# Optimization experiments

Hardware: AMD Instinct MI355X
Metric: run time of the kernel (lower is better)

## Reference

```python
import jax, jax.numpy as jnp
import numpy as np


def setup_inputs() -> dict:
    key = jax.random.key(0)
    k1, k2 = jax.random.split(key)
    N, D, C = 65536, 512, 64
    embeddings = jax.random.normal(k1, (N, D), dtype=jnp.float32)
    labels = jax.random.randint(k2, (N,), 0, C, dtype=jnp.int64)
    return {"embeddings": embeddings, "labels": labels, "num_classes": C}


def reference(embeddings, labels, num_classes):
    # Per-class mean (prototypes) via segment reductions. Labels are assumed
    # to be 0..C-1 with all classes present, so unique(labels) == arange(C)
    # and local_labels == labels (faithful to the torch loop in that regime).
    ones = jnp.ones(labels.shape, dtype=embeddings.dtype)
    counts = jax.ops.segment_sum(ones, labels, num_segments=num_classes)  # [C]
    sums = jax.ops.segment_sum(embeddings, labels, num_segments=num_classes)  # [C, D]
    prototypes = sums / counts[:, None]

    # Euclidean cdist: ||e||^2 + ||p||^2 - 2 e.p^T, clamped for numerical safety
    e2 = jnp.sum(embeddings * embeddings, axis=1, keepdims=True)  # [N, 1]
    p2 = jnp.sum(prototypes * prototypes, axis=1)  # [C]
    cross = embeddings @ prototypes.T  # [N, C]
    d2 = jnp.maximum(e2 + p2[None, :] - 2.0 * cross, 1e-12)
    logits = -jnp.sqrt(d2)  # [N, C], negative distances

    log_probs = jax.nn.log_softmax(logits, axis=1)
    n = labels.shape[0]
    nll = -log_probs[jnp.arange(n), labels]
    loss = jnp.mean(nll)
    accuracy = jnp.mean((jnp.argmax(logits, axis=1) == labels).astype(jnp.float32))
    return (loss, accuracy)
```

## Files before the change

kernel.cpp:

```cpp
#include <hip/hip_runtime.h>
#include <math.h>

#define NROWS 65536
#define DIM   512
#define NCLS  64
#define CCAP  1280

typedef __attribute__((ext_vector_type(4))) float f32x4;
typedef __attribute__((ext_vector_type(8))) short s16x8;

#define WS_PROTOSUM 0
#define WS_CURSORS  32768
#define WS_LOSS     32832
#define WS_ACC      32833
#define WS_DONE     32834
#define WS_P2       32836
#define WS_PERM     32912
#define WS_PBF      114944
#define MEMSET_WORDS 32835

static __device__ __forceinline__ unsigned short f2bf(float f) {
    unsigned int u = __float_as_uint(f);
    u += 0x7FFF + ((u >> 16) & 1);
    return (unsigned short)(u >> 16);
}
static __device__ __forceinline__ float bf2f(unsigned short h) {
    return __uint_as_float(((unsigned int)h) << 16);
}

__global__ __launch_bounds__(256) void k_scatter(const int* __restrict__ labels,
                                                 int* __restrict__ cursors,
                                                 int* __restrict__ perm) {
    __shared__ int lh[NCLS], lb[NCLS];
    int t = threadIdx.x;
    if (t < NCLS) lh[t] = 0;
    __syncthreads();
    int i = blockIdx.x * 256 + t;
    int lab = labels[i];
    int rank = atomicAdd(&lh[lab], 1);
    __syncthreads();
    if (t < NCLS) lb[t] = atomicAdd(&cursors[t], lh[t]);
    __syncthreads();
    int pos = lb[lab] + rank;
    if (pos < CCAP) perm[lab * CCAP + pos] = i;
}

__global__ __launch_bounds__(256) void k_psum(const float* __restrict__ emb,
                                              const int* __restrict__ cursors,
                                              const int* __restrict__ perm,
                                              float* __restrict__ protoSum) {
    __shared__ int permS[CCAP];
    __shared__ float4 red[256];
    int t   = threadIdx.x;
    int c   = blockIdx.x >> 5;
    int sub = blockIdx.x & 31;
    int dc  = sub & 3;
    int rs  = sub >> 2;
    int tl  = t & 31;
    int g   = t >> 5;

    int cnt = cursors[c];
    int n = (cnt < CCAP) ? cnt : CCAP;
    for (int i = t; i < n; i += 256) permS[i] = perm[c * CCAP + i];
    __syncthreads();

    const float4* eb = (const float4*)emb + dc * 32 + tl;
    float4 acc = make_float4(0.f, 0.f, 0.f, 0.f);
#pragma unroll 4
    for (int i = rs * 8 + g; i < n; i += 64) {
        int r = permS[i];
        float4 v = eb[(size_t)r * 128];
        acc.x += v.x; acc.y += v.y; acc.z += v.z; acc.w += v.w;
    }
    red[t] = acc;
    __syncthreads();
    if (t < 32) {
        float4 s = red[t];
#pragma unroll
        for (int gg = 1; gg < 8; ++gg) {
            float4 v = red[gg * 32 + t];
            s.x += v.x; s.y += v.y; s.z += v.z; s.w += v.w;
        }
        float* dst = &protoSum[(size_t)c * DIM + dc * 128 + t * 4];
        atomicAdd(dst + 0, s.x);
        atomicAdd(dst + 1, s.y);
        atomicAdd(dst + 2, s.z);
        atomicAdd(dst + 3, s.w);
    }
}

__global__ __launch_bounds__(512) void k_protofin(const float* __restrict__ protoSum,
                                                  const int* __restrict__ cursors,
                                                  unsigned short* __restrict__ pBf,
                                                  float* __restrict__ p2) {
    int c = blockIdx.x, d = threadIdx.x;
    float mean = protoSum[(size_t)c * DIM + d] / (float)cursors[c];
    unsigned short mb = f2bf(mean);
    int kc = d >> 5, quad = (d >> 3) & 3, j = d & 7;
    int nt = c >> 4, l15 = c & 15;
    pBf[(size_t)(((kc * 4 + quad) * 4 + nt) * 16 + l15) * 8 + j] = mb;
    float mf = bf2f(mb);
    float sq = mf * mf;
#pragma unroll
    for (int o = 32; o > 0; o >>= 1) sq += __shfl_down(sq, o, 64);
    __shared__ float red[8];
    if ((d & 63) == 0) red[d >> 6] = sq;
    __syncthreads();
    if (d == 0) {
        float ss = 0.f;
#pragma unroll
        for (int w = 0; w < 8; ++w) ss += red[w];
        p2[c] = ss;
    }
}

#define LROWS 64
#define LGRID (NROWS / LROWS)
__global__ __launch_bounds__(256) void k_logits(const float* __restrict__ emb,
                                                const int* __restrict__ labels,
                                                const unsigned short* __restrict__ pBf,
                                                const float* __restrict__ p2,
                                                float* __restrict__ lossAcc,
                                                float* __restrict__ accAcc,
                                                unsigned int* __restrict__ doneCnt,
                                                float* __restrict__ out) {
    __shared__ __align__(16) unsigned short Asm[2][LROWS * 36];
    __shared__ float e2s[LROWS];
    __shared__ float rb[8];

    int t    = threadIdx.x;
    int lane = t & 63;
    int wv   = t >> 6;
    int quad = lane >> 4;
    int l15  = lane & 15;
    int rbase = blockIdx.x * LROWS;

    f32x4 acc[4];
#pragma unroll
    for (int nt = 0; nt < 4; ++nt) acc[nt] = (f32x4){0.f, 0.f, 0.f, 0.f};
    float e2a0 = 0.f, e2a1 = 0.f;

    const float4* emb4 = (const float4*)(emb + (size_t)rbase * DIM);
    int row0 = t >> 3, j0 = t & 7;
    int row1 = 32 + row0;

    float4 g0 = emb4[(size_t)row0 * 128 + j0];
    float4 g1 = emb4[(size_t)row1 * 128 + j0];
    s16x8 bf[4];
#pragma unroll
    for (int nt = 0; nt < 4; ++nt)
        bf[nt] = *(const s16x8*)(pBf + (size_t)((quad * 4 + nt) * 16 + l15) * 8);

#pragma unroll 4
    for (int kc = 0; kc < 16; ++kc) {
        int buf = kc & 1;
        e2a0 += g0.x * g0.x + g0.y * g0.y + g0.z * g0.z + g0.w * g0.w;
        e2a1 += g1.x * g1.x + g1.y * g1.y + g1.z * g1.z + g1.w * g1.w;
        ushort4 h0, h1;
        h0.x = f2bf(g0.x); h0.y = f2bf(g0.y); h0.z = f2bf(g0.z); h0.w = f2bf(g0.w);
        h1.x = f2bf(g1.x); h1.y = f2bf(g1.y); h1.z = f2bf(g1.z); h1.w = f2bf(g1.w);
        *(ushort4*)&Asm[buf][row0 * 36 + j0 * 4] = h0;
        *(ushort4*)&Asm[buf][row1 * 36 + j0 * 4] = h1;

        float4 n0, n1; s16x8 nb[4];
        if (kc < 15) {
            n0 = emb4[(size_t)row0 * 128 + (kc + 1) * 8 + j0];
            n1 = emb4[(size_t)row1 * 128 + (kc + 1) * 8 + j0];
#pragma unroll
            for (int nt = 0; nt < 4; ++nt)
                nb[nt] = *(const s16x8*)(pBf +
                    (size_t)((((kc + 1) * 4 + quad) * 4 + nt) * 16 + l15) * 8);
        }

        asm volatile("s_waitcnt lgkmcnt(0)\n\ts_barrier" ::: "memory");

        s16x8 a = *(const s16x8*)&Asm[buf][(wv * 16 + l15) * 36 + quad * 8];
#pragma unroll
        for (int nt = 0; nt < 4; ++nt)
            acc[nt] = __builtin_amdgcn_mfma_f32_16x16x32_bf16(a, bf[nt], acc[nt], 0, 0, 0);

        g0 = n0; g1 = n1;
#pragma unroll
        for (int nt = 0; nt < 4; ++nt) bf[nt] = nb[nt];
    }

    float v0 = e2a0;
    v0 += __shfl_xor(v0, 1, 64); v0 += __shfl_xor(v0, 2, 64); v0 += __shfl_xor(v0, 4, 64);
    float v1 = e2a1;
    v1 += __shfl_xor(v1, 1, 64); v1 += __shfl_xor(v1, 2, 64); v1 += __shfl_xor(v1, 4, 64);
    if ((lane & 7) == 0) {
        e2s[wv * 8 + (lane >> 3)]      = v0;
        e2s[32 + wv * 8 + (lane >> 3)] = v1;
    }
    __syncthreads();

    float nlls = 0.f, corr = 0.f;
#pragma unroll
    for (int reg = 0; reg < 4; ++reg) {
        int rloc = wv * 16 + quad * 4 + reg;
        float e2v = e2s[rloc];
        float lg[4];
#pragma unroll
        for (int nt = 0; nt < 4; ++nt) {
            float d2 = e2v + p2[nt * 16 + l15] - 2.f * acc[nt][reg];
            d2 = fmaxf(d2, 1e-12f);
            lg[nt] = -sqrtf(d2);
        }
        float mv = lg[0]; int mc = l15;
#pragma unroll
        for (int nt = 1; nt < 4; ++nt) {
            int cix = nt * 16 + l15;
            if (lg[nt] > mv) { mv = lg[nt]; mc = cix; }
        }
#pragma unroll
        for (int o = 1; o < 16; o <<= 1) {
            float mo = __shfl_xor(mv, o, 64);
            int   co = __shfl_xor(mc, o, 64);
            if (mo > mv || (mo == mv && co < mc)) { mv = mo; mc = co; }
        }
        int lab = labels[rbase + rloc];
        float se = 0.f, ll = 0.f;
#pragma unroll
        for (int nt = 0; nt < 4; ++nt) se += __expf(lg[nt] - mv);
        if ((lab & 15) == l15) ll = lg[lab >> 4];
#pragma unroll
        for (int o = 1; o < 16; o <<= 1) {
            se += __shfl_xor(se, o, 64);
            ll += __shfl_xor(ll, o, 64);
        }
        if (l15 == 0) {
            nlls += __logf(se) + mv - ll;
            corr += (mc == lab) ? 1.f : 0.f;
        }
    }
#pragma unroll
    for (int o = 1; o < 64; o <<= 1) {
        nlls += __shfl_xor(nlls, o, 64);
        corr += __shfl_xor(corr, o, 64);
    }
    if (lane == 0) { rb[wv] = nlls; rb[4 + wv] = corr; }
    __syncthreads();
    if (t == 0) {
        atomicAdd(lossAcc, rb[0] + rb[1] + rb[2] + rb[3]);
        atomicAdd(accAcc, rb[4] + rb[5] + rb[6] + rb[7]);
        __threadfence();
        unsigned int tk = atomicAdd(doneCnt, 1u);
        if (tk == LGRID - 1) {
            float ls  = atomicAdd(lossAcc, 0.f);
            float as_ = atomicAdd(accAcc, 0.f);
            out[0] = ls * (1.f / NROWS);
            out[1] = as_ * (1.f / NROWS);
        }
    }
}

extern "C" void kernel_launch(void* const* d_in, const int* in_sizes, int n_in,
                              void* d_out, int out_size, void* d_ws, size_t ws_size,
                              hipStream_t stream) {
    const float* emb    = (const float*)d_in[0];
    const int*   labels = (const int*)d_in[1];
    float* out = (float*)d_out;

    float* wsf = (float*)d_ws;
    int*   wsi = (int*)d_ws;
    float*          protoSum = wsf + WS_PROTOSUM;
    int*            cursors  = wsi + WS_CURSORS;
    float*          lossAcc  = wsf + WS_LOSS;
    float*          accAcc   = wsf + WS_ACC;
    unsigned int*   doneCnt  = (unsigned int*)(wsi + WS_DONE);
    float*          p2       = wsf + WS_P2;
    int*            perm     = wsi + WS_PERM;
    unsigned short* pBf      = (unsigned short*)(wsf + WS_PBF);

    hipMemsetAsync(d_ws, 0, MEMSET_WORDS * sizeof(int), stream);

    k_scatter<<<NROWS / 256, 256, 0, stream>>>(labels, cursors, perm);
    k_psum<<<NCLS * 32, 256, 0, stream>>>(emb, cursors, perm, protoSum);
    k_protofin<<<NCLS, 512, 0, stream>>>(protoSum, cursors, pBf, p2);
    k_logits<<<LGRID, 256, 0, stream>>>(emb, labels, pBf, p2,
                                        lossAcc, accAcc, doneCnt, out);
}
```

Baseline: 271.0 us.

## Load MFMA A-fragments directly from global memory, dropping LDS staging and barriers

Each lane now reads its own two float4 chunks of the embedding row straight from global memory, converts them to bf16 in registers and feeds them to the MFMA. This removes the shared-memory staging buffer and the per-iteration barrier. The row-norm reduction becomes a cross-quad shuffle. The cost is less coalesced global access (32-byte pieces per lane across 16 rows) and the loss of the explicit double-buffered prefetch of embeddings and prototype fragments, so latency hiding now depends on unrolling.

```diff
diff --git a/kernel.cpp b/kernel.cpp
--- a/kernel.cpp
+++ b/kernel.cpp
@@ -124,7 +124,6 @@
                                                 float* __restrict__ accAcc,
                                                 unsigned int* __restrict__ doneCnt,
                                                 float* __restrict__ out) {
-    __shared__ __align__(16) unsigned short Asm[2][LROWS * 36];
     __shared__ float e2s[LROWS];
     __shared__ float rb[8];
 
@@ -134,64 +133,35 @@
     int quad = lane >> 4;
     int l15  = lane & 15;
     int rbase = blockIdx.x * LROWS;
+    int row   = wv * 16 + l15;
 
     f32x4 acc[4];
 #pragma unroll
     for (int nt = 0; nt < 4; ++nt) acc[nt] = (f32x4){0.f, 0.f, 0.f, 0.f};
-    float e2a0 = 0.f, e2a1 = 0.f;
-
-    const float4* emb4 = (const float4*)(emb + (size_t)rbase * DIM);
-    int row0 = t >> 3, j0 = t & 7;
-    int row1 = 32 + row0;
-
-    float4 g0 = emb4[(size_t)row0 * 128 + j0];
-    float4 g1 = emb4[(size_t)row1 * 128 + j0];
-    s16x8 bf[4];
-#pragma unroll
-    for (int nt = 0; nt < 4; ++nt)
-        bf[nt] = *(const s16x8*)(pBf + (size_t)((quad * 4 + nt) * 16 + l15) * 8);
+    float e2a = 0.f;
+
+    const float4* rp = (const float4*)(emb + (size_t)(rbase + row) * DIM) + quad * 2;
+    const s16x8*  bp = (const s16x8*)pBf + quad * 64 + l15;
 
 #pragma unroll 4
     for (int kc = 0; kc < 16; ++kc) {
-        int buf = kc & 1;
-        e2a0 += g0.x * g0.x + g0.y * g0.y + g0.z * g0.z + g0.w * g0.w;
-        e2a1 += g1.x * g1.x + g1.y * g1.y + g1.z * g1.z + g1.w * g1.w;
-        ushort4 h0, h1;
-        h0.x = f2bf(g0.x); h0.y = f2bf(g0.y); h0.z = f2bf(g0.z); h0.w = f2bf(g0.w);
-        h1.x = f2bf(g1.x); h1.y = f2bf(g1.y); h1.z = f2bf(g1.z); h1.w = f2bf(g1.w);
-        *(ushort4*)&Asm[buf][row0 * 36 + j0 * 4] = h0;
-        *(ushort4*)&Asm[buf][row1 * 36 + j0 * 4] = h1;
-
-        float4 n0, n1; s16x8 nb[4];
-        if (kc < 15) {
-            n0 = emb4[(size_t)row0 * 128 + (kc + 1) * 8 + j0];
-            n1 = emb4[(size_t)row1 * 128 + (kc + 1) * 8 + j0];
-#pragma unroll
-            for (int nt = 0; nt < 4; ++nt)
-                nb[nt] = *(const s16x8*)(pBf +
-                    (size_t)((((kc + 1) * 4 + quad) * 4 + nt) * 16 + l15) * 8);
-        }
-
-        asm volatile("s_waitcnt lgkmcnt(0)\n\ts_barrier" ::: "memory");
-
-        s16x8 a = *(const s16x8*)&Asm[buf][(wv * 16 + l15) * 36 + quad * 8];
-#pragma unroll
-        for (int nt = 0; nt < 4; ++nt)
-            acc[nt] = __builtin_amdgcn_mfma_f32_16x16x32_bf16(a, bf[nt], acc[nt], 0, 0, 0);
-
-        g0 = n0; g1 = n1;
-#pragma unroll
-        for (int nt = 0; nt < 4; ++nt) bf[nt] = nb[nt];
-    }
-
-    float v0 = e2a0;
-    v0 += __shfl_xor(v0, 1, 64); v0 += __shfl_xor(v0, 2, 64); v0 += __shfl_xor(v0, 4, 64);
-    float v1 = e2a1;
-    v1 += __shfl_xor(v1, 1, 64); v1 += __shfl_xor(v1, 2, 64); v1 += __shfl_xor(v1, 4, 64);
-    if ((lane & 7) == 0) {
-        e2s[wv * 8 + (lane >> 3)]      = v0;
-        e2s[32 + wv * 8 + (lane >> 3)] = v1;
-    }
+        float4 g0 = rp[kc * 8];
+        float4 g1 = rp[kc * 8 + 1];
+        e2a += g0.x * g0.x + g0.y * g0.y + g0.z * g0.z + g0.w * g0.w
+             + g1.x * g1.x + g1.y * g1.y + g1.z * g1.z + g1.w * g1.w;
+        s16x8 a;
+        a[0] = f2bf(g0.x); a[1] = f2bf(g0.y); a[2] = f2bf(g0.z); a[3] = f2bf(g0.w);
+        a[4] = f2bf(g1.x); a[5] = f2bf(g1.y); a[6] = f2bf(g1.z); a[7] = f2bf(g1.w);
+#pragma unroll
+        for (int nt = 0; nt < 4; ++nt) {
+            s16x8 b = bp[kc * 256 + nt * 16];
+            acc[nt] = __builtin_amdgcn_mfma_f32_16x16x32_bf16(a, b, acc[nt], 0, 0, 0);
+        }
+    }
+
+    e2a += __shfl_xor(e2a, 16, 64);
+    e2a += __shfl_xor(e2a, 32, 64);
+    if (quad == 0) e2s[row] = e2a;
     __syncthreads();
 
     float nlls = 0.f, corr = 0.f;
```

Measured after the change: 279.8 us. 3.3% more time.
